# Kernel optimization log

Hardware: AMD Instinct MI355X
Metric: run time of the kernel (lower is better)

## Reference

```python
import jax, jax.numpy as jnp
import numpy as np

N = 100_000      # atoms (nodes)
E = 1_600_000    # directed edges
F_IN = 89        # atom feature dim
H = 128          # hidden dim
P = 20_000       # polyhedra (N/P = 5 atoms each)
C = 500          # crystals (P/C = 40 polyhedra each)
OUT = 1
EPS = 1e-5


def setup_inputs() -> dict:
    key = jax.random.key(0)
    ks = jax.random.split(key, 10)
    x = jax.random.normal(ks[0], (N, F_IN), jnp.float32)
    edge_index = jax.random.randint(ks[1], (2, E), 0, N)
    # sorted segment ids guaranteeing non-empty segments (faithful to PyG Batch layout)
    batch = jnp.repeat(jnp.arange(P), N // P)          # node -> polyhedron
    crystal_ids = jnp.repeat(jnp.arange(C), P // C)    # polyhedron -> crystal
    # GCNConv weights (glorot-ish) and biases; conv0 maps 89->128, convs 1..4 map 128->128
    W0 = jax.random.normal(ks[2], (F_IN, H), jnp.float32) * (1.0 / np.sqrt(F_IN))
    Ws = jax.random.normal(ks[3], (4, H, H), jnp.float32) * (1.0 / np.sqrt(H))
    bs = jnp.zeros((5, H), jnp.float32)
    # 5 BatchNorm layers
    gammas = jnp.ones((5, H), jnp.float32)
    betas = jnp.zeros((5, H), jnp.float32)
    # predictor MLP
    Wp1 = jax.random.normal(ks[4], (H, H), jnp.float32) * (1.0 / np.sqrt(H))
    bp1 = jnp.zeros((H,), jnp.float32)
    Wp2 = jax.random.normal(ks[5], (H, OUT), jnp.float32) * (1.0 / np.sqrt(H))
    bp2 = jnp.zeros((OUT,), jnp.float32)
    return dict(x=x, edge_index=edge_index, batch=batch, crystal_ids=crystal_ids,
                W0=W0, Ws=Ws, bs=bs, gammas=gammas, betas=betas,
                Wp1=Wp1, bp1=bp1, Wp2=Wp2, bp2=bp2)


def _bn(h, g, b):
    # BatchNorm1d, training mode: biased batch statistics over nodes
    mu = jnp.mean(h, axis=0)
    var = jnp.var(h, axis=0)
    return g * (h - mu) * jax.lax.rsqrt(var + EPS) + b


def reference(x, edge_index, batch, crystal_ids, W0, Ws, bs, gammas, betas, Wp1, bp1, Wp2, bp2):
    # --- GCN normalization with self-loops (shared by all 5 convs) ---
    loops = jnp.arange(N)
    src = jnp.concatenate([edge_index[0], loops])   # [E+N]
    dst = jnp.concatenate([edge_index[1], loops])
    deg = jax.ops.segment_sum(jnp.ones_like(src, jnp.float32), dst, num_segments=N)
    dinv = jnp.where(deg > 0, jax.lax.rsqrt(deg), 0.0)
    norm = (dinv[src] * dinv[dst])[:, None]          # [E+N, 1]

    def conv(h, W, b):
        m = h @ W                                    # [N, H]
        agg = jax.ops.segment_sum(m[src] * norm, dst, num_segments=N)
        return agg + b

    h = jax.nn.relu(_bn(conv(x, W0, bs[0]), gammas[0], betas[0]))
    for i in range(4):
        h = jax.nn.relu(_bn(conv(h, Ws[i], bs[i + 1]), gammas[i + 1], betas[i + 1]))

    # global_mean_pool over polyhedra
    cnt_p = jax.ops.segment_sum(jnp.ones((N,), jnp.float32), batch, num_segments=P)
    poly = jax.ops.segment_sum(h, batch, num_segments=P) / cnt_p[:, None]

    # per-crystal mean of polyhedron reps (vectorized form of the Python loop)
    cnt_c = jax.ops.segment_sum(jnp.ones((P,), jnp.float32), crystal_ids, num_segments=C)
    crys = jax.ops.segment_sum(poly, crystal_ids, num_segments=C) / cnt_c[:, None]

    # predictor MLP (Dropout is identity at inference)
    pred = jax.nn.relu(crys @ Wp1 + bp1) @ Wp2 + bp2   # [C, 1]
    return pred
```

## Files before the change

### kernel.cpp

```cpp
#include <hip/hip_runtime.h>

#define N_ATOMS 100000
#define N_EDGES 1600000
#define F_INDIM 89
#define N_CRYS  500
#define EPSBN   1e-5f
#define DRANGE  12500
#define RBLK    250
#define NSB     400
#define CAPSEG  28160
#define SEGCH   110

typedef unsigned short u16;
typedef unsigned int   u32;
typedef unsigned long long u64;
typedef __attribute__((ext_vector_type(8))) short short8;
typedef __attribute__((ext_vector_type(4))) float f32x4;
typedef __attribute__((ext_vector_type(4))) unsigned int u32x4;

__device__ __forceinline__ float bf2f(u16 u){ union{u32 i; float f;} v; v.i=((u32)u)<<16; return v.f; }
__device__ __forceinline__ float bflo(u32 u){ union{u32 i; float f;} v; v.i=u<<16; return v.f; }
__device__ __forceinline__ float bfhi(u32 u){ union{u32 i; float f;} v; v.i=u&0xffff0000u; return v.f; }
__device__ __forceinline__ u16 f2bf(float f){
  u32 x=__float_as_uint(f);
  return (u16)((x + 0x7fffu + ((x>>16)&1u))>>16);
}
__device__ __forceinline__ u32 pack2(float a, float b){ return (u32)f2bf(a) | ((u32)f2bf(b)<<16); }
__device__ __forceinline__ float ldf(const void* p, int i, int m){
  return m ? ((const float*)p)[i] : bf2f(((const u16*)p)[i]);
}
__device__ __forceinline__ int fpmode(const void* gammas){ return (((const u16*)gammas)[0]==0) ? 1 : 0; }

__global__ void k_bucket(const int* __restrict__ ei, u64* __restrict__ bkt, int* __restrict__ bcnt){
  __shared__ int lcnt[8], lbase[8];
  int t = threadIdx.x;
  int seg = blockIdx.x & 7;
  int e = blockIdx.x*256 + t;
  if (t < 8) lcnt[t] = 0;
  __syncthreads();
  int d=0, s=0, rr=0, li=0;
  bool valid = (e < N_EDGES);
  if (valid){
    d = ei[N_EDGES+e]; if ((u32)d >= N_ATOMS) d = 0;
    s = ei[e];         if ((u32)s >= N_ATOMS) s = 0;
    rr = d / DRANGE;
    li = atomicAdd(&lcnt[rr], 1);
  }
  __syncthreads();
  if (t < 8) lbase[t] = atomicAdd(&bcnt[seg*64 + t], lcnt[t]);
  __syncthreads();
  if (valid){
    bkt[(size_t)(seg*8 + rr)*CAPSEG + lbase[rr] + li] = ((u64)(u32)d << 32) | (u32)s;
  }
}

__global__ void k_count2(const u64* __restrict__ bkt, const int* __restrict__ bcnt,
                         int* __restrict__ degi){
  int rr  = blockIdx.x & 7;
  int rest = blockIdx.x >> 3;
  int seg = rest & 7, ch = rest >> 3;
  int i = ch*256 + threadIdx.x;
  if (i >= bcnt[seg*64 + rr]) return;
  int d = (int)(bkt[(size_t)(seg*8 + rr)*CAPSEG + i] >> 32);
  atomicAdd(&degi[d], 1);
}

__global__ void k_hist(const int* __restrict__ degi, int* __restrict__ hist, int* __restrict__ blockHist){
  __shared__ int lh[256];
  int t = threadIdx.x, b = blockIdx.x;
  lh[t] = 0; __syncthreads();
  if (t < RBLK){
    int dg = degi[b*RBLK + t];
    atomicAdd(&lh[dg>255?255:dg], 1);
  }
  __syncthreads();
  blockHist[b*256 + t] = lh[t];
  if (lh[t]) atomicAdd(&hist[(b/50)*256 + t], lh[t]);
}

__global__ void k_hist_scan(int* __restrict__ hist){
  __shared__ int s[256];
  int R = blockIdx.x, t = threadIdx.x;
  int own = hist[R*256+t]; s[t] = own; __syncthreads();
  for (int k=1;k<256;k<<=1){ int a=(t>=k)?s[t-k]:0; __syncthreads(); s[t]+=a; __syncthreads(); }
  hist[R*256+t] = s[t] - own;
}

__global__ __launch_bounds__(64) void k_blockoff(const int* __restrict__ blockHist, const int* __restrict__ binBase,
                                                 int* __restrict__ blockOff){
  int bid = blockIdx.x;
  int c = bid & 255, R = bid >> 8;
  int t = threadIdx.x;
  int own = (t<50) ? blockHist[(R*50+t)*256 + c] : 0;
  int v = own;
  #pragma unroll
  for (int k=1;k<64;k<<=1){ int u = __shfl_up(v, k, 64); if (t>=k) v += u; }
  if (t<50) blockOff[(R*50+t)*256 + c] = R*DRANGE + binBase[R*256 + c] + (v - own);
}

__global__ void k_rank(const int* __restrict__ degi, const int* __restrict__ blockOff,
                       int* __restrict__ nodeAt, int* __restrict__ rankOf,
                       float* __restrict__ dinv, float* __restrict__ dinvR){
  __shared__ int boff[256];
  __shared__ int cnt[256];
  int b = blockIdx.x, t = threadIdx.x;
  boff[t] = blockOff[b*256 + t];
  cnt[t] = 0;
  __syncthreads();
  if (t >= RBLK) return;
  int n = b*RBLK + t;
  int dg = degi[n];
  int cd = dg>255?255:dg;
  int li = atomicAdd(&cnt[cd], 1);
  int r = boff[cd] + li;
  nodeAt[r] = n; rankOf[n] = r;
  float di = rsqrtf((float)(dg + 1));
  dinv[n] = di; dinvR[r] = di;
}

__global__ __launch_bounds__(256) void k_scan_partial(const int* __restrict__ degi, const int* __restrict__ nodeAt,
                                                      int* __restrict__ bsum){
  int b=blockIdx.x, t=threadIdx.x;
  int s=0;
  #pragma unroll
  for (int j=0;j<4;j++){
    int i=b*1024 + j*256 + t;
    if(i<N_ATOMS){
      int dg = degi[nodeAt[i]];
      s += (dg+3)&~3;
    }
  }
  __shared__ int red[256];
  red[t]=s; __syncthreads();
  for (int k=128;k>0;k>>=1){ if(t<k) red[t]+=red[t+k]; __syncthreads(); }
  if (t==0) bsum[b]=red[0];
}

__global__ void k_scan_bsum(int* __restrict__ bsum, int nb){
  __shared__ int s[128];
  int t=threadIdx.x;
  int own = (t<nb)? bsum[t]:0;
  s[t]=own; __syncthreads();
  for (int k=1;k<128;k<<=1){ int a=(t>=k)?s[t-k]:0; __syncthreads(); s[t]+=a; __syncthreads(); }
  if (t<nb) bsum[t]=s[t]-own;
}

__global__ __launch_bounds__(256) void k_scan_write(const int* __restrict__ degi, const int* __restrict__ nodeAt,
                                                    const int* __restrict__ bsum,
                                                    int* __restrict__ off, u32* __restrict__ csrS){
  int b=blockIdx.x, t=threadIdx.x;
  int base=b*1024+t*4;
  int v[4], s=0;
  #pragma unroll
  for (int j=0;j<4;j++){ int i=base+j; v[j]=(i<N_ATOMS)?((degi[nodeAt[i]]+3)&~3):0; s+=v[j]; }
  __shared__ int ts[256];
  ts[t]=s; __syncthreads();
  for (int k=1;k<256;k<<=1){ int a=(t>=k)?ts[t-k]:0; __syncthreads(); ts[t]+=a; __syncthreads(); }
  int run = ts[t]-s + bsum[b];
  #pragma unroll
  for (int j=0;j<4;j++){
    int i=base+j;
    if (i<=N_ATOMS) off[i]=run;
    if (i<N_ATOMS){
      int dg = degi[nodeAt[i]];
      for (int q=dg; q<v[j]; q++) csrS[run+q] = (u32)N_ATOMS;
    }
    run+=v[j];
  }
}

__global__ void k_fill2(const u64* __restrict__ bkt, const int* __restrict__ bcnt,
                        const int* __restrict__ off, const int* __restrict__ rankOf,
                        int* __restrict__ cursor, u32* __restrict__ csrS){
  int rr  = blockIdx.x & 7;
  int rest = blockIdx.x >> 3;
  int seg = rest & 7, ch = rest >> 3;
  int i = ch*256 + threadIdx.x;
  if (i >= bcnt[seg*64 + rr]) return;
  u64 v = bkt[(size_t)(seg*8 + rr)*CAPSEG + i];
  int d = (int)(v >> 32);
  int s = (int)(u32)v;
  int rk = rankOf[d];
  int p = off[rk] + atomicAdd(&cursor[rk], 1);
  csrS[p] = (u32)s;
}

__global__ void k_packW(const void* __restrict__ W0, const void* __restrict__ Ws,
                        const void* __restrict__ gammas, u16* __restrict__ dst){
  int L    = blockIdx.x >> 3;
  int tid  = (blockIdx.x & 7)*256 + threadIdx.x;
  int K    = (L==0) ? F_INDIM : 128;
  int Kpad = (L==0) ? 96 : 128;
  if (tid >= (Kpad/32)*8*64) return;
  const void* W = (L==0) ? W0 : Ws;
  int woff = (L==0) ? 0 : (L-1)*128*128;
  int fp32m = fpmode(gammas);
  int lane = tid & 63, sc = tid >> 6;
  int c = sc & 7, s = sc >> 3;
  u16 vals[8];
  #pragma unroll
  for (int j=0;j<8;j++){
    int k  = s*32 + (lane>>4)*8 + j;
    int ch = c*16 + (lane&15);
    float v = (k<K) ? ldf(W, woff + k*128 + ch, fp32m) : 0.f;
    vals[j] = f2bf(v);
  }
  u16* out = dst + (size_t)L*16384;
  *(ushort4*)&out[tid*8]   = *(const ushort4*)&vals[0];
  *(ushort4*)&out[tid*8+4] = *(const ushort4*)&vals[4];
}

#define AROW 136
__global__ __launch_bounds__(256) void k_gemm_mfma(const u16* __restrict__ inA, const void* __restrict__ inX,
                                                   int K, int Kpad, const u16* __restrict__ Wpk,
                                                   const float* __restrict__ statsPrev, int useAct,
                                                   const float* __restrict__ dinv,
                                                   u16* __restrict__ mout,
                                                   const void* __restrict__ gammas,
                                                   const void* __restrict__ betas, int goff){
  __shared__ __align__(16) u16 Al[128*AROW];
  __shared__ float cl[256];
  const int t = threadIdx.x, lane = t & 63, w = t >> 6;
  const int tile = blockIdx.x * 128;

  if (useAct){
    if (t < 128){
      int fp32m = fpmode(gammas);
      float mu  = statsPrev[t] * (1.f/N_ATOMS);
      float var = statsPrev[128+t] * (1.f/N_ATOMS) - mu*mu;
      if (var < 0.f) var = 0.f;
      float sc = ldf(gammas, goff+t, fp32m) / sqrtf(var + EPSBN);
      cl[t]     = sc;
      cl[128+t] = ldf(betas, goff+t, fp32m) - sc*mu;
    }
    __syncthreads();
    const uint4* HA4 = (const uint4*)inA;
    for (int idx=t; idx<128*16; idx+=256){
      int node = idx>>4, q = idx&15;
      int gn = tile+node;
      uint4 v = (gn<N_ATOMS) ? HA4[((size_t)(q>>2)*(N_ATOMS+1) + gn)*4 + (q&3)] : make_uint4(0,0,0,0);
      int kk = q*8;
      u16 r[8];
      r[0]=f2bf(fmaxf(fmaf(cl[kk+0], bflo(v.x), cl[128+kk+0]),0.f));
      r[1]=f2bf(fmaxf(fmaf(cl[kk+1], bfhi(v.x), cl[128+kk+1]),0.f));
      r[2]=f2bf(fmaxf(fmaf(cl[kk+2], bflo(v.y), cl[128+kk+2]),0.f));
      r[3]=f2bf(fmaxf(fmaf(cl[kk+3], bfhi(v.y), cl[128+kk+3]),0.f));
      r[4]=f2bf(fmaxf(fmaf(cl[kk+4], bflo(v.z), cl[128+kk+4]),0.f));
      r[5]=f2bf(fmaxf(fmaf(cl[kk+5], bfhi(v.z), cl[128+kk+5]),0.f));
      r[6]=f2bf(fmaxf(fmaf(cl[kk+6], bflo(v.w), cl[128+kk+6]),0.f));
      r[7]=f2bf(fmaxf(fmaf(cl[kk+7], bfhi(v.w), cl[128+kk+7]),0.f));
      *(uint4*)&Al[node*AROW + kk] = *(const uint4*)&r[0];
    }
  } else {
    int fp32m = fpmode(gammas);
    for (int idx=t; idx<128*96; idx+=256){
      int node = idx/96, kk = idx - node*96;
      int gn = tile+node;
      float v = (kk<K && gn<N_ATOMS) ? ldf(inX, gn*K+kk, fp32m) : 0.f;
      Al[node*AROW + kk] = f2bf(v);
    }
  }
  __syncthreads();

  f32x4 acc[2][8];
  #pragma unroll
  for (int rr=0;rr<2;rr++)
    #pragma unroll
    for (int c=0;c<8;c++) acc[rr][c] = (f32x4){0.f,0.f,0.f,0.f};
  const int row = lane & 15, quad = lane >> 4;

  const int nstep = Kpad >> 5;
  for (int s=0; s<nstep; ++s){
    short8 a0 = *(const short8*)&Al[(w*32+row)*AROW    + s*32 + quad*8];
    short8 a1 = *(const short8*)&Al[(w*32+16+row)*AROW + s*32 + quad*8];
    #pragma unroll
    for (int c=0;c<8;c++){
      short8 b = *(const short8*)&Wpk[(size_t)((s*8+c)*64 + lane)*8];
      acc[0][c] = __builtin_amdgcn_mfma_f32_16x16x32_bf16(a0, b, acc[0][c], 0, 0, 0);
      acc[1][c] = __builtin_amdgcn_mfma_f32_16x16x32_bf16(a1, b, acc[1][c], 0, 0, 0);
    }
  }
  __syncthreads();
  float di[2][4];
  #pragma unroll
  for (int rr=0;rr<2;rr++)
    #pragma unroll
    for (int r=0;r<4;r++){
      int gn = tile + w*32 + rr*16 + quad*4 + r;
      di[rr][r] = (gn<N_ATOMS) ? dinv[gn] : 0.f;
    }
  #pragma unroll
  for (int rr=0;rr<2;rr++)
    #pragma unroll
    for (int c=0;c<8;c++)
      #pragma unroll
      for (int r=0;r<4;r++){
        int node = w*32 + rr*16 + quad*4 + r, ch = c*16 + row;
        Al[node*AROW + ch] = f2bf(di[rr][r]*acc[rr][c][r]);
      }
  __syncthreads();
  for (int idx=t; idx<2048; idx+=256){
    int blk = idx>>9, rem = idx&511, node = rem>>2, part = rem&3;
    int gn = tile+node;
    if (gn < N_ATOMS){
      uint4 v = *(const uint4*)&Al[node*AROW + blk*32 + part*8];
      *(uint4*)&mout[((size_t)blk*(N_ATOMS+1) + gn)*32 + part*8] = v;
    }
  }
  if (blockIdx.x == gridDim.x-1 && t < 16){
    int blk = t>>2, part = t&3;
    *(uint4*)&mout[((size_t)blk*(N_ATOMS+1) + N_ATOMS)*32 + part*8] = make_uint4(0,0,0,0);
  }
}

#define ACC8(r) do{ a[0]+=bflo(r.x); a[1]+=bfhi(r.x); a[2]+=bflo(r.y); a[3]+=bfhi(r.y); \
                    a[4]+=bflo(r.z); a[5]+=bfhi(r.z); a[6]+=bflo(r.w); a[7]+=bfhi(r.w);}while(0)
__global__ __launch_bounds__(256) void k_agg(const u16* __restrict__ m_, const u32* __restrict__ csrS,
                                             const int* __restrict__ off, const int* __restrict__ nodeAt,
                                             const float* __restrict__ dinvR,
                                             u16* __restrict__ agg_, float* __restrict__ stats){
  const int t = threadIdx.x, lane = t & 63, w = t >> 6;
  const int par = lane & 3, p = lane >> 2;
  const int cls = blockIdx.x & 7;
  const int slice = cls >> 1, half = cls & 1;
  const int r = half*50000 + (int)(blockIdx.x >> 3)*64 + w*16 + p;
  const int rlim = half*50000 + 50000;

  const uint4* m4   = (const uint4*)m_ + (size_t)slice*(N_ATOMS+1)*4;
  uint4*       agg4 = (uint4*)agg_     + (size_t)slice*(N_ATOMS+1)*4;

  float a[8], q8[8];
  #pragma unroll
  for (int i=0;i<8;i++){ a[i]=0.f; q8[i]=0.f; }

  if (r < rlim){
    int n = nodeAt[r];
    uint4 sv = m4[(size_t)n*4 + par];
    ACC8(sv);
    int e   = off[r];
    int end = off[r+1];
    if ((end - e) & 4){
      u32x4 iv = *(const u32x4*)(csrS+e);
      uint4 g0 = m4[(size_t)iv[0]*4 + par];
      uint4 g1 = m4[(size_t)iv[1]*4 + par];
      uint4 g2 = m4[(size_t)iv[2]*4 + par];
      uint4 g3 = m4[(size_t)iv[3]*4 + par];
      ACC8(g0); ACC8(g1); ACC8(g2); ACC8(g3);
      e += 4;
    }
    if (e < end){
      u32x4 i0 = *(const u32x4*)(csrS+e), i1 = *(const u32x4*)(csrS+e+4);
      uint4 A0 = m4[(size_t)i0[0]*4 + par];
      uint4 A1 = m4[(size_t)i0[1]*4 + par];
      uint4 A2 = m4[(size_t)i0[2]*4 + par];
      uint4 A3 = m4[(size_t)i0[3]*4 + par];
      uint4 A4 = m4[(size_t)i1[0]*4 + par];
      uint4 A5 = m4[(size_t)i1[1]*4 + par];
      uint4 A6 = m4[(size_t)i1[2]*4 + par];
      uint4 A7 = m4[(size_t)i1[3]*4 + par];
      e += 8;
      bool more = (e < end);
      while (true){
        uint4 B0,B1,B2,B3,B4,B5,B6,B7;
        if (more){
          u32x4 j0 = *(const u32x4*)(csrS+e), j1 = *(const u32x4*)(csrS+e+4);
          B0 = m4[(size_t)j0[0]*4 + par];
          B1 = m4[(size_t)j0[1]*4 + par];
          B2 = m4[(size_t)j0[2]*4 + par];
          B3 = m4[(size_t)j0[3]*4 + par];
          B4 = m4[(size_t)j1[0]*4 + par];
          B5 = m4[(size_t)j1[1]*4 + par];
          B6 = m4[(size_t)j1[2]*4 + par];
          B7 = m4[(size_t)j1[3]*4 + par];
          e += 8;
        }
        ACC8(A0); ACC8(A1); ACC8(A2); ACC8(A3);
        ACC8(A4); ACC8(A5); ACC8(A6); ACC8(A7);
        if (!more) break;
        A0=B0; A1=B1; A2=B2; A3=B3; A4=B4; A5=B5; A6=B6; A7=B7;
        more = (e < end);
      }
    }
    float di = dinvR[r];
    #pragma unroll
    for (int i=0;i<8;i++){ a[i]*=di; q8[i]=a[i]*a[i]; }
    u32x4 o;
    o[0] = pack2(a[0],a[1]); o[1] = pack2(a[2],a[3]);
    o[2] = pack2(a[4],a[5]); o[3] = pack2(a[6],a[7]);
    __builtin_nontemporal_store(o, (u32x4*)&agg4[(size_t)n*4 + par]);
  }
  #pragma unroll
  for (int i=0;i<8;i++){
    float s = a[i], q = q8[i];
    s += __shfl_xor(s, 4, 64);  q += __shfl_xor(q, 4, 64);
    s += __shfl_xor(s, 8, 64);  q += __shfl_xor(q, 8, 64);
    s += __shfl_xor(s, 16, 64); q += __shfl_xor(q, 16, 64);
    s += __shfl_xor(s, 32, 64); q += __shfl_xor(q, 32, 64);
    a[i]=s; q8[i]=q;
  }
  __shared__ float sred[4][64];
  if (lane < 4){
    #pragma unroll
    for (int i=0;i<8;i++){ sred[w][par*8+i]=a[i]; sred[w][32+par*8+i]=q8[i]; }
  }
  __syncthreads();
  if (t < 64){
    float v = sred[0][t]+sred[1][t]+sred[2][t]+sred[3][t];
    int ch = slice*32 + (t & 31);
    atomicAdd(&stats[(t<32 ? ch : 128+ch)], v);
  }
}

__global__ __launch_bounds__(128) void k_pool_mlp(const u16* __restrict__ agg, const float* __restrict__ stats4,
                                                  const void* __restrict__ gammas, const void* __restrict__ betas,
                                                  const void* __restrict__ Wp1, const void* __restrict__ bp1,
                                                  const void* __restrict__ Wp2, const void* __restrict__ bp2,
                                                  void* __restrict__ out){
  int c = blockIdx.x, t = threadIdx.x;
  int fp32m = fpmode(gammas);
  float mu  = stats4[t] * (1.f/N_ATOMS);
  float var = stats4[128+t] * (1.f/N_ATOMS) - mu*mu;
  if (var < 0.f) var = 0.f;
  float sc = ldf(gammas, 512+t, fp32m) / sqrtf(var + EPSBN);
  float tb = ldf(betas, 512+t, fp32m) - sc*mu;
  float sum = 0.f;
  const u16* base = agg + ((size_t)(t>>5)*(N_ATOMS+1) + (size_t)c*200)*32 + (t&31);
  for (int i=0;i<200;i++) sum += fmaxf(fmaf(sc, bf2f(base[(size_t)i*32]), tb), 0.f);
  __shared__ float cr[128];
  cr[t] = sum * (1.f/200.f);
  __syncthreads();
  float hj = ldf(bp1, t, fp32m);
  for (int k=0;k<128;k++) hj = fmaf(cr[k], ldf(Wp1, k*128+t, fp32m), hj);
  hj = fmaxf(hj, 0.f);
  __shared__ float red[128];
  red[t] = hj * ldf(Wp2, t, fp32m);
  __syncthreads();
  for (int s=64;s>0;s>>=1){ if (t<s) red[t]+=red[t+s]; __syncthreads(); }
  if (t==0){
    float r = red[0] + ldf(bp2, 0, fp32m);
    if (fp32m) ((float*)out)[c] = r;
    else       ((u16*) out)[c]  = f2bf(r);
  }
}

extern "C" void kernel_launch(void* const* d_in, const int* in_sizes, int n_in,
                              void* d_out, int out_size, void* d_ws, size_t ws_size,
                              hipStream_t stream){
  const void* x      = d_in[0];
  const int*  ei     = (const int*)d_in[1];
  const void* W0     = d_in[4];
  const void* Ws     = d_in[5];
  const void* gammas = d_in[7];
  const void* betas  = d_in[8];
  const void* Wp1    = d_in[9];
  const void* bp1    = d_in[10];
  const void* Wp2    = d_in[11];
  const void* bp2    = d_in[12];
  (void)in_sizes; (void)n_in; (void)out_size; (void)ws_size;

  char* w = (char*)d_ws;
  size_t o = 0;
  auto take = [&](size_t bytes)->char*{ char* p = w+o; o = (o+bytes+255)&~(size_t)255; return p; };
  int*   off    = (int*)  take((size_t)(N_ATOMS+1)*4);
  float* dinv   = (float*)take((size_t)N_ATOMS*4);
  u32*   csrS   = (u32*)  take((size_t)(N_EDGES+4*N_ATOMS)*4);
  u16*   HA     = (u16*)  take((size_t)(N_ATOMS+1)*128*2);
  u16*   HB     = (u16*)  take((size_t)(N_ATOMS+1)*128*2);
  float* stats5 = (float*)take(5*256*4);
  int*   bsum   = (int*)  take(1024*4);
  u16*   Wpk    = (u16*)  take((size_t)5*16384*2);
  int*   nodeAt = (int*)  take((size_t)N_ATOMS*4);
  float* dinvR  = (float*)take((size_t)N_ATOMS*4);
  int* degi      = (int*)HB;
  int* hist      = (int*)((char*)HB + 400128);
  int* cursor    = (int*)((char*)HB + 408320);
  int* bcnt      = (int*)((char*)HB + 808320);
  int* rankOf    = (int*)((char*)HB + 810496);
  int* blockHist = (int*)((char*)HB + 1210496);
  int* blockOff  = (int*)((char*)HB + 1620096);
  u64* bkt       = (u64*)((char*)HB + 2097152);

  k_packW<<<40, 256, 0, stream>>>(W0, Ws, gammas, Wpk);

  hipMemsetAsync(degi, 0, 810368, stream);
  const int echunks = (N_EDGES+255)/256;
  const int bgrid   = SEGCH*8*8;
  k_bucket<<<echunks, 256, 0, stream>>>(ei, bkt, bcnt);
  k_count2<<<bgrid, 256, 0, stream>>>(bkt, bcnt, degi);
  k_hist <<<NSB, 256, 0, stream>>>(degi, hist, blockHist);
  k_hist_scan<<<8, 256, 0, stream>>>(hist);
  k_blockoff<<<8*256, 64, 0, stream>>>(blockHist, hist, blockOff);
  k_rank <<<NSB, 256, 0, stream>>>(degi, blockOff, nodeAt, rankOf, dinv, dinvR);
  const int nb = (N_ATOMS+1023)/1024;
  k_scan_partial<<<nb, 256, 0, stream>>>(degi, nodeAt, bsum);
  k_scan_bsum   <<<1, 128, 0, stream>>>(bsum, nb);
  k_scan_write  <<<nb, 256, 0, stream>>>(degi, nodeAt, bsum, off, csrS);
  k_fill2<<<bgrid, 256, 0, stream>>>(bkt, bcnt, off, rankOf, cursor, csrS);
  hipMemsetAsync(stats5, 0, 5*256*4, stream);

  const int gemm_grid = (N_ATOMS+127)/128;
  const int agg_grid  = ((50000+63)/64)*8;
  for (int L=0; L<5; ++L){
    const int Kpad = (L==0) ? 96 : 128;
    const int K    = (L==0) ? F_INDIM : 128;
    const float* statsPrev = (L==0) ? stats5 : (stats5 + (size_t)(L-1)*256);
    k_gemm_mfma<<<gemm_grid, 256, 0, stream>>>(HA, x, K, Kpad, Wpk + (size_t)L*16384,
                                               statsPrev, (L==0)?0:1, dinv, HB,
                                               gammas, betas, (L-1)*128);
    k_agg <<<agg_grid, 256, 0, stream>>>(HB, csrS, off, nodeAt, dinvR, HA, stats5 + (size_t)L*256);
  }
  k_pool_mlp<<<N_CRYS, 128, 0, stream>>>(HA, stats5 + 4*256, gammas, betas,
                                         Wp1, bp1, Wp2, bp2, d_out);
}
```

Baseline: 774.4 us.

## Replace atomic CSR scatter with two-pass grouped bucketing through shared memory

Replaces the per-edge global-atomic CSR fill with two passes. The first pass bins edges into groups of 128 ranked nodes in shared memory and writes them contiguously. The second pass builds each group's CSR slice in an LDS image, padding included, and copies it out with vector stores. This removes scattered global atomics and random 4-byte writes, at the cost of an extra intermediate buffer pass and shared-memory pressure.

```diff
diff --git a/kernel.cpp b/kernel.cpp
--- a/kernel.cpp
+++ b/kernel.cpp
@@ -9,7 +9,11 @@
 #define RBLK    250
 #define NSB     400
 #define CAPSEG  28160
-#define SEGCH   110
+#define GRP     128
+#define NGRP    782
+#define B1E     2048
+#define NBIN    104
+#define IMGMAX  12288
 
 typedef unsigned short u16;
 typedef unsigned int   u32;
@@ -147,7 +151,7 @@
 
 __global__ __launch_bounds__(256) void k_scan_write(const int* __restrict__ degi, const int* __restrict__ nodeAt,
                                                     const int* __restrict__ bsum,
-                                                    int* __restrict__ off, u32* __restrict__ csrS){
+                                                    int* __restrict__ off){
   int b=blockIdx.x, t=threadIdx.x;
   int base=b*1024+t*4;
   int v[4], s=0;
@@ -161,28 +165,97 @@
   for (int j=0;j<4;j++){
     int i=base+j;
     if (i<=N_ATOMS) off[i]=run;
-    if (i<N_ATOMS){
-      int dg = degi[nodeAt[i]];
-      for (int q=dg; q<v[j]; q++) csrS[run+q] = (u32)N_ATOMS;
-    }
     run+=v[j];
   }
 }
 
-__global__ void k_fill2(const u64* __restrict__ bkt, const int* __restrict__ bcnt,
-                        const int* __restrict__ off, const int* __restrict__ rankOf,
-                        int* __restrict__ cursor, u32* __restrict__ csrS){
-  int rr  = blockIdx.x & 7;
-  int rest = blockIdx.x >> 3;
-  int seg = rest & 7, ch = rest >> 3;
-  int i = ch*256 + threadIdx.x;
-  if (i >= bcnt[seg*64 + rr]) return;
-  u64 v = bkt[(size_t)(seg*8 + rr)*CAPSEG + i];
-  int d = (int)(v >> 32);
-  int s = (int)(u32)v;
-  int rk = rankOf[d];
-  int p = off[rk] + atomicAdd(&cursor[rk], 1);
-  csrS[p] = (u32)s;
+__global__ __launch_bounds__(256) void k_group(const u64* __restrict__ bkt, const int* __restrict__ bcnt,
+                                               const int* __restrict__ rankOf, const int* __restrict__ off,
+                                               int* __restrict__ cnt2, u64* __restrict__ bkt2){
+  __shared__ int lcnt[NBIN], loff[NBIN], gb[NBIN];
+  __shared__ u64 lval[B1E];
+  __shared__ int ldst[B1E];
+  const int t = threadIdx.x;
+  const int rr = blockIdx.x & 7;
+  const int rest = blockIdx.x >> 3;
+  const int seg = rest & 7, ch = rest >> 3;
+  const int cnt = bcnt[seg*64 + rr];
+  const int e0 = ch*B1E;
+  int nloc = cnt - e0; if (nloc < 0) nloc = 0; if (nloc > B1E) nloc = B1E;
+  const int g0 = (rr*DRANGE) >> 7;
+  if (t < NBIN){ lcnt[t] = 0; }
+  __syncthreads();
+  const u64* src = bkt + (size_t)(seg*8 + rr)*CAPSEG + e0;
+  int rk8[8], s8[8], sl8[8];
+  #pragma unroll
+  for (int j=0;j<8;j++){
+    int i = j*256 + t;
+    rk8[j] = -1;
+    if (i < nloc){
+      u64 v = src[i];
+      int rk = rankOf[(int)(v>>32)];
+      rk8[j] = rk; s8[j] = (int)(u32)v;
+      sl8[j] = atomicAdd(&lcnt[(rk>>7) - g0], 1);
+    }
+  }
+  __syncthreads();
+  if (t == 0){
+    int run = 0;
+    for (int b=0;b<NBIN;b++){ loff[b] = run; run += lcnt[b]; }
+  }
+  __syncthreads();
+  if (t < NBIN && lcnt[t] > 0){
+    int g = g0 + t;
+    gb[t] = off[g*GRP] + atomicAdd(&cnt2[g], lcnt[t]);
+  }
+  __syncthreads();
+  #pragma unroll
+  for (int j=0;j<8;j++){
+    if (rk8[j] >= 0){
+      int rel = (rk8[j]>>7) - g0;
+      int p = loff[rel] + sl8[j];
+      lval[p] = ((u64)(u32)rk8[j] << 32) | (u32)s8[j];
+      ldst[p] = gb[rel] + sl8[j];
+    }
+  }
+  __syncthreads();
+  for (int i=t; i<nloc; i+=256)
+    bkt2[ldst[i]] = lval[i];
+}
+
+__global__ __launch_bounds__(256) void k_csr(const u64* __restrict__ bkt2, const int* __restrict__ cnt2,
+                                             const int* __restrict__ off, u32* __restrict__ csrS){
+  __shared__ u32 img[IMGMAX];
+  __shared__ int lcur[GRP];
+  const int g = blockIdx.x, t = threadIdx.x;
+  const int r0 = g*GRP;
+  const int r1 = (r0+GRP < N_ATOMS) ? r0+GRP : N_ATOMS;
+  const int base = off[r0];
+  const int size = off[r1] - base;
+  const int n = cnt2[g];
+  if (size <= IMGMAX){
+    for (int i=t; i<size; i+=256) img[i] = (u32)N_ATOMS;
+    if (t < r1-r0) lcur[t] = off[r0+t] - base;
+    __syncthreads();
+    for (int i=t; i<n; i+=256){
+      u64 v = bkt2[(size_t)base + i];
+      int p = atomicAdd(&lcur[(int)(v>>32) - r0], 1);
+      img[p] = (u32)v;
+    }
+    __syncthreads();
+    uint4* c4 = (uint4*)(csrS + base);
+    const uint4* i4 = (const uint4*)img;
+    for (int i=t; i<(size>>2); i+=256) c4[i] = i4[i];
+  } else {
+    if (t < r1-r0) lcur[t] = off[r0+t];
+    for (int i=t; i<size; i+=256) csrS[base+i] = (u32)N_ATOMS;
+    __syncthreads();
+    for (int i=t; i<n; i+=256){
+      u64 v = bkt2[(size_t)base + i];
+      int p = atomicAdd(&lcur[(int)(v>>32) - r0], 1);
+      csrS[p] = (u32)v;
+    }
+  }
 }
 
 __global__ void k_packW(const void* __restrict__ W0, const void* __restrict__ Ws,
@@ -473,18 +546,20 @@
   float* dinvR  = (float*)take((size_t)N_ATOMS*4);
   int* degi      = (int*)HB;
   int* hist      = (int*)((char*)HB + 400128);
-  int* cursor    = (int*)((char*)HB + 408320);
-  int* bcnt      = (int*)((char*)HB + 808320);
+  int* bcnt      = (int*)((char*)HB + 408320);
+  int* cnt2      = (int*)((char*)HB + 410368);
   int* rankOf    = (int*)((char*)HB + 810496);
   int* blockHist = (int*)((char*)HB + 1210496);
   int* blockOff  = (int*)((char*)HB + 1620096);
   u64* bkt       = (u64*)((char*)HB + 2097152);
+  u64* bkt2      = (u64*)HA;
 
   k_packW<<<40, 256, 0, stream>>>(W0, Ws, gammas, Wpk);
 
-  hipMemsetAsync(degi, 0, 810368, stream);
+  hipMemsetAsync(degi, 0, 413568, stream);
   const int echunks = (N_EDGES+255)/256;
-  const int bgrid   = SEGCH*8*8;
+  const int bgrid   = ((CAPSEG+255)/256)*8*8;
+  const int ggrid   = ((CAPSEG+B1E-1)/B1E)*8*8;
   k_bucket<<<echunks, 256, 0, stream>>>(ei, bkt, bcnt);
   k_count2<<<bgrid, 256, 0, stream>>>(bkt, bcnt, degi);
   k_hist <<<NSB, 256, 0, stream>>>(degi, hist, blockHist);
@@ -494,8 +569,9 @@
   const int nb = (N_ATOMS+1023)/1024;
   k_scan_partial<<<nb, 256, 0, stream>>>(degi, nodeAt, bsum);
   k_scan_bsum   <<<1, 128, 0, stream>>>(bsum, nb);
-  k_scan_write  <<<nb, 256, 0, stream>>>(degi, nodeAt, bsum, off, csrS);
-  k_fill2<<<bgrid, 256, 0, stream>>>(bkt, bcnt, off, rankOf, cursor, csrS);
+  k_scan_write  <<<nb, 256, 0, stream>>>(degi, nodeAt, bsum, off);
+  k_group<<<ggrid, 256, 0, stream>>>(bkt, bcnt, rankOf, off, cnt2, bkt2);
+  k_csr  <<<NGRP, 256, 0, stream>>>(bkt2, cnt2, off, csrS);
   hipMemsetAsync(stats5, 0, 5*256*4, stream);
 
   const int gemm_grid = (N_ATOMS+127)/128;
```

Result: faster. 726.9 us (-6.1%).
